# Kernel optimization log

Hardware: AMD Instinct MI355X
Metric: run time of the kernel (lower is better)

Reference implementation:

```python
import jax, jax.numpy as jnp
import numpy as np

ALPHA = 0.25
GAMMA = 2.0
VAR = jnp.array([0.1, 0.1, 0.2, 0.2, 0.1, 0.1, 0.2, 0.2], dtype=jnp.float32)


def calc_iou(a, b):
    # a: [A,4] anchors, b: [M,4] gt boxes -> IoU [A,M]
    area = (b[:, 2] - b[:, 0]) * (b[:, 3] - b[:, 1])
    iw = jnp.maximum(jnp.minimum(a[:, 2:3], b[:, 2]) - jnp.maximum(a[:, 0:1], b[:, 0]), 0.0)
    ih = jnp.maximum(jnp.minimum(a[:, 3:4], b[:, 3]) - jnp.maximum(a[:, 1:2], b[:, 1]), 0.0)
    ua = jnp.maximum(((a[:, 2] - a[:, 0]) * (a[:, 3] - a[:, 1]))[:, None] + area - iw * ih, 1e-8)
    return iw * ih / ua


def _per_sample(cls_p, reg, anchor, ann1, ann2):
    A = anchor.shape[0]
    M = ann1.shape[0]
    C = cls_p.shape[1]
    clsp = jnp.clip(cls_p, 1e-4, 1.0 - 1e-4)
    iou = calc_iou(anchor, ann1[:, :4])               # [A,M]
    bto = jnp.max(iou, axis=1)                        # best_truth_overlap [A]
    bti = jnp.argmax(iou, axis=1)                     # best_truth_idx [A]
    bpi = jnp.argmax(iou, axis=0)                     # best_prior_idx [M]
    bto = bto.at[bpi].set(2.0)
    owner = jnp.full((A,), -1, jnp.int32).at[bpi].max(jnp.arange(M, dtype=jnp.int32))
    bti = jnp.where(owner >= 0, owner, bti.astype(jnp.int32))
    pos = bto >= 0.5
    neg = bto < 0.4
    assigned = ann1[bti]                              # [A,6]
    labels = assigned[:, 4].astype(jnp.int32)
    onehot = jax.nn.one_hot(labels, C, dtype=clsp.dtype)
    targets = jnp.where(neg[:, None], 0.0, -1.0)
    targets = jnp.where(pos[:, None], onehot, targets)
    af = jnp.where(targets == 1.0, ALPHA, 1.0 - ALPHA)
    fw = af * jnp.where(targets == 1.0, 1.0 - clsp, clsp) ** GAMMA
    bce = -(targets * jnp.log(clsp) + (1.0 - targets) * jnp.log(1.0 - clsp))
    cls_loss = jnp.where(targets != -1.0, fw * bce, 0.0)
    npos = jnp.sum(pos).astype(clsp.dtype)
    cls_out = cls_loss.sum() / jnp.maximum(npos, 1.0)

    aw = anchor[:, 2] - anchor[:, 0]
    ah = anchor[:, 3] - anchor[:, 1]
    acx = anchor[:, 0] + 0.5 * aw
    acy = anchor[:, 1] + 0.5 * ah
    # track-id first-match between frames (replaces nested python loops)
    match = assigned[:, 5][:, None] == ann2[:, 5][None, :]   # [A,M2]
    has = jnp.any(match, axis=1)
    first = jnp.argmax(match, axis=1)
    ann_next = jnp.where(has[:, None], ann2[first], 0.0)     # [A,6]
    gw0 = assigned[:, 2] - assigned[:, 0]
    gh0 = assigned[:, 3] - assigned[:, 1]
    gcx = assigned[:, 0] + 0.5 * gw0
    gcy = assigned[:, 1] + 0.5 * gh0
    gw = jnp.maximum(gw0, 1.0)
    gh = jnp.maximum(gh0, 1.0)
    nw0 = ann_next[:, 2] - ann_next[:, 0]
    nh0 = ann_next[:, 3] - ann_next[:, 1]
    ncx = ann_next[:, 0] + 0.5 * nw0
    ncy = ann_next[:, 1] + 0.5 * nh0
    nw = jnp.maximum(nw0, 1.0)
    nh = jnp.maximum(nh0, 1.0)
    t = jnp.stack([
        (gcx - acx) / aw, (gcy - acy) / ah, jnp.log(gw / aw), jnp.log(gh / ah),
        (ncx - acx) / aw, (ncy - acy) / ah, jnp.log(nw / aw), jnp.log(nh / ah)
    ], axis=1) / VAR                                          # [A,8]
    reg_mask = jnp.concatenate([
        jnp.ones((A, 4), clsp.dtype),
        jnp.broadcast_to(has[:, None], (A, 4)).astype(clsp.dtype)
    ], axis=1)
    diff = jnp.abs(t - reg) * reg_mask
    hub = jnp.where(diff <= 1.0 / 9.0, 0.5 * 9.0 * diff ** 2, diff - 0.5 / 9.0)
    reg_out = jnp.sum(hub * pos[:, None].astype(clsp.dtype)) / jnp.maximum(npos * 8.0, 1.0)
    return cls_out, reg_out


def reference(classifications, regressions, anchors, annotations1, annotations2):
    cl, rl = jax.vmap(_per_sample, in_axes=(0, 0, None, 0, 0))(
        classifications, regressions, anchors[0], annotations1, annotations2)
    return jnp.mean(cl, keepdims=True), jnp.mean(rl, keepdims=True)


def setup_inputs() -> dict:
    key = jax.random.key(0)
    ks = jax.random.split(key, 10)
    B, A, C, M = 8, 100000, 80, 32
    IMG = 512.0

    def rand_boxes(k, prefix):
        k1, k2 = jax.random.split(k)
        ctr = jax.random.uniform(k1, prefix + (2,), jnp.float32, 0.0, IMG)
        wh = jax.random.uniform(k2, prefix + (2,), jnp.float32, 16.0, 128.0)
        return jnp.concatenate([ctr - 0.5 * wh, ctr + 0.5 * wh], axis=-1)

    anchors = rand_boxes(ks[0], (1, A))
    classifications = jax.random.uniform(ks[1], (B, A, C), jnp.float32)
    regressions = jax.random.normal(ks[2], (B, A, 8), jnp.float32) * 0.1

    def make_ann(kb, ki):
        boxes = rand_boxes(kb, (B, M))
        lbl = jax.random.randint(ki, (B, M, 1), 0, C).astype(jnp.float32)
        tid = jax.random.randint(jax.random.fold_in(ki, 1), (B, M, 1), 0, 40).astype(jnp.float32)
        return jnp.concatenate([boxes, lbl, tid], axis=-1)

    annotations1 = make_ann(ks[3], ks[4])
    annotations2 = make_ann(ks[5], ks[6])
    return {"classifications": classifications, "regressions": regressions,
            "anchors": anchors, "annotations1": annotations1, "annotations2": annotations2}
```

## Files before the change

kernel.cpp:

```cpp
#include <hip/hip_runtime.h>

typedef unsigned long long ull;
typedef float nvec4 __attribute__((ext_vector_type(4)));

#define MMAX 128

__global__ void k_init(ull* __restrict__ bpi, int* __restrict__ npos,
                       float* __restrict__ cls_sum, float* __restrict__ reg_sum,
                       int BM, int B) {
    int i = blockIdx.x * blockDim.x + threadIdx.x;
    if (i < BM) bpi[i] = 0ull;
    if (i < B) { npos[i] = 0; cls_sum[i] = 0.f; reg_sum[i] = 0.f; }
}

__global__ void k_iou(const float* __restrict__ anchors, const float* __restrict__ ann1,
                      float* __restrict__ bto, int* __restrict__ bti, ull* __restrict__ bpi,
                      int A, int M) {
    __shared__ float s_box[MMAX][4];
    __shared__ float s_area[MMAX];
    __shared__ ull s_part[4][MMAX];
    const int b = blockIdx.y;
    const int tid = threadIdx.x;
    for (int i = tid; i < M; i += blockDim.x) {
        const float* g = ann1 + ((size_t)b * M + i) * 6;
        float x1 = g[0], y1 = g[1], x2 = g[2], y2 = g[3];
        s_box[i][0] = x1; s_box[i][1] = y1; s_box[i][2] = x2; s_box[i][3] = y2;
        s_area[i] = (x2 - x1) * (y2 - y1);
    }
    __syncthreads();

    const int base = blockIdx.x * (blockDim.x * 4);
    float ax1[4], ay1[4], ax2[4], ay2[4], aar[4];
    int aidx[4]; bool val[4];
#pragma unroll
    for (int u = 0; u < 4; ++u) {
        int a = base + u * blockDim.x + tid;
        aidx[u] = a; val[u] = (a < A);
        float4 av = make_float4(0.f, 0.f, 0.f, 0.f);
        if (val[u]) av = ((const float4*)anchors)[a];
        ax1[u] = av.x; ay1[u] = av.y; ax2[u] = av.z; ay2[u] = av.w;
        aar[u] = (av.z - av.x) * (av.w - av.y);
    }
    float best[4] = {-1.f, -1.f, -1.f, -1.f};
    int bestj[4] = {0, 0, 0, 0};
    const int lane = tid & 63, wid = tid >> 6;

    for (int j = 0; j < M; ++j) {
        float bx1 = s_box[j][0], by1 = s_box[j][1], bx2 = s_box[j][2], by2 = s_box[j][3];
        float bar = s_area[j];
        ull key = 0ull;
#pragma unroll
        for (int u = 0; u < 4; ++u) {
            float iw = fmaxf(fminf(ax2[u], bx2) - fmaxf(ax1[u], bx1), 0.f);
            float ih = fmaxf(fminf(ay2[u], by2) - fmaxf(ay1[u], by1), 0.f);
            float inter = iw * ih;
            float ua = fmaxf(aar[u] + bar - inter, 1e-8f);
            float iou = inter / ua;
            if (val[u]) {
                if (iou > best[u]) { best[u] = iou; bestj[u] = j; }
                ull k2 = (((ull)__float_as_uint(iou)) << 32) | (ull)(0xFFFFFFFFu - (unsigned)aidx[u]);
                if (k2 > key) key = k2;
            }
        }
#pragma unroll
        for (int off = 32; off > 0; off >>= 1) {
            ull o = __shfl_down(key, off);
            if (o > key) key = o;
        }
        if (lane == 0) s_part[wid][j] = key;
    }
#pragma unroll
    for (int u = 0; u < 4; ++u) {
        if (val[u]) {
            bto[(size_t)b * A + aidx[u]] = best[u];
            bti[(size_t)b * A + aidx[u]] = bestj[u];
        }
    }
    __syncthreads();
    for (int j = tid; j < M; j += blockDim.x) {
        ull key = s_part[0][j];
        if (s_part[1][j] > key) key = s_part[1][j];
        if (s_part[2][j] > key) key = s_part[2][j];
        if (s_part[3][j] > key) key = s_part[3][j];
        atomicMax(&bpi[(size_t)b * M + j], key);
    }
}

__global__ void k_force(const ull* __restrict__ bpi, float* __restrict__ bto,
                        int* __restrict__ bti, int A, int M, int B) {
    int b = blockIdx.x * blockDim.x + threadIdx.x;
    if (b >= B) return;
    for (int j = 0; j < M; ++j) {
        ull key = bpi[(size_t)b * M + j];
        unsigned a = 0xFFFFFFFFu - (unsigned)(key & 0xFFFFFFFFull);
        bto[(size_t)b * A + a] = 2.0f;
        bti[(size_t)b * A + a] = j;
    }
}

template <int C4C>
__global__ void k_cls(const float* __restrict__ cls, const float* __restrict__ ann1,
                      const float* __restrict__ bto, const int* __restrict__ bti,
                      float* __restrict__ cls_sum, int A, int c4_rt, int M) {
    const int c4 = (C4C > 0) ? C4C : c4_rt;
    const int b = blockIdx.y;
    const int N4 = A * c4;
    const nvec4* cb = (const nvec4*)(cls + (size_t)b * A * (c4 * 4));
    const float* btob = bto + (size_t)b * A;
    const int* btib = bti + (size_t)b * A;
    const float* ann1b = ann1 + (size_t)b * M * 6;
    float lsum = 0.f;
    const int stride = gridDim.x * blockDim.x;
    for (int i = blockIdx.x * blockDim.x + threadIdx.x; i < N4; i += stride) {
        int a = i / c4;
        int c0 = (i - a * c4) * 4;
        float v = btob[a];
        bool pos = (v >= 0.5f), neg = (v < 0.4f);
        if (pos || neg) {
            nvec4 x = __builtin_nontemporal_load(&cb[i]);
            int label = -1;
            if (pos) label = (int)ann1b[btib[a] * 6 + 4];
            float xs[4] = {x[0], x[1], x[2], x[3]};
#pragma unroll
            for (int k = 0; k < 4; ++k) {
                float p = fminf(fmaxf(xs[k], 1e-4f), 1.0f - 1e-4f);
                if (pos && (c0 + k) == label) {
                    float q = 1.f - p;
                    lsum += 0.25f * q * q * (-__logf(p));
                } else {
                    lsum += 0.75f * p * p * (-__logf(1.f - p));
                }
            }
        }
    }
#pragma unroll
    for (int off = 32; off > 0; off >>= 1) lsum += __shfl_down(lsum, off);
    __shared__ float s_red[4];
    if ((threadIdx.x & 63) == 0) s_red[threadIdx.x >> 6] = lsum;
    __syncthreads();
    if (threadIdx.x == 0)
        atomicAdd(&cls_sum[b], s_red[0] + s_red[1] + s_red[2] + s_red[3]);
}

__global__ void k_reg(const float* __restrict__ anchors, const float* __restrict__ ann1,
                      const float* __restrict__ ann2, const float* __restrict__ regs,
                      const float* __restrict__ bto, const int* __restrict__ bti,
                      float* __restrict__ reg_sum, int* __restrict__ npos,
                      int A, int M, int M2) {
    __shared__ float s_a1[MMAX * 6];
    __shared__ float s_a2[MMAX * 6];
    const int b = blockIdx.y;
    const int tid = threadIdx.x;
    for (int i = tid; i < M * 6; i += blockDim.x) s_a1[i] = ann1[(size_t)b * M * 6 + i];
    for (int i = tid; i < M2 * 6; i += blockDim.x) s_a2[i] = ann2[(size_t)b * M2 * 6 + i];
    __syncthreads();

    const int a = blockIdx.x * blockDim.x + tid;
    float sum = 0.f;
    int cnt = 0;
    if (a < A) {
        float v = bto[(size_t)b * A + a];
        if (v >= 0.5f) {
            cnt = 1;
            const int ji = bti[(size_t)b * A + a];
            const float* as = &s_a1[ji * 6];
            float4 av = ((const float4*)anchors)[a];
            float aw = av.z - av.x, ah = av.w - av.y;
            float acx = av.x + 0.5f * aw, acy = av.y + 0.5f * ah;
            float gw0 = as[2] - as[0], gh0 = as[3] - as[1];
            float gcx = as[0] + 0.5f * gw0, gcy = as[1] + 0.5f * gh0;
            float gw = fmaxf(gw0, 1.f), gh = fmaxf(gh0, 1.f);
            float t[8];
            t[0] = ((gcx - acx) / aw) / 0.1f;
            t[1] = ((gcy - acy) / ah) / 0.1f;
            t[2] = __logf(gw / aw) / 0.2f;
            t[3] = __logf(gh / ah) / 0.2f;
            int nterm = 4;
            float tid5 = as[5];
            int first = -1;
            for (int j2 = 0; j2 < M2; ++j2) {
                if (s_a2[j2 * 6 + 5] == tid5) { first = j2; break; }
            }
            if (first >= 0) {
                const float* ns = &s_a2[first * 6];
                float nw0 = ns[2] - ns[0], nh0 = ns[3] - ns[1];
                float ncx = ns[0] + 0.5f * nw0, ncy = ns[1] + 0.5f * nh0;
                float nw = fmaxf(nw0, 1.f), nh = fmaxf(nh0, 1.f);
                t[4] = ((ncx - acx) / aw) / 0.1f;
                t[5] = ((ncy - acy) / ah) / 0.1f;
                t[6] = __logf(nw / aw) / 0.2f;
                t[7] = __logf(nh / ah) / 0.2f;
                nterm = 8;
            }
            const float* rg = regs + ((size_t)b * A + a) * 8;
            for (int k = 0; k < nterm; ++k) {
                float d = fabsf(t[k] - __builtin_nontemporal_load(&rg[k]));
                sum += (d <= (1.0f / 9.0f)) ? (4.5f * d * d) : (d - (0.5f / 9.0f));
            }
        }
    }
#pragma unroll
    for (int off = 32; off > 0; off >>= 1) {
        sum += __shfl_down(sum, off);
        cnt += __shfl_down(cnt, off);
    }
    __shared__ float s_rs[4];
    __shared__ int s_rc[4];
    if ((tid & 63) == 0) { s_rs[tid >> 6] = sum; s_rc[tid >> 6] = cnt; }
    __syncthreads();
    if (tid == 0) {
        atomicAdd(&reg_sum[b], s_rs[0] + s_rs[1] + s_rs[2] + s_rs[3]);
        atomicAdd(&npos[b], s_rc[0] + s_rc[1] + s_rc[2] + s_rc[3]);
    }
}

__global__ void k_final(const float* __restrict__ cls_sum, const float* __restrict__ reg_sum,
                        const int* __restrict__ npos, float* __restrict__ out, int B) {
    if (blockIdx.x == 0 && threadIdx.x == 0) {
        float c = 0.f, r = 0.f;
        for (int b = 0; b < B; ++b) {
            float np_ = (float)npos[b];
            c += cls_sum[b] / fmaxf(np_, 1.f);
            r += reg_sum[b] / fmaxf(np_ * 8.f, 1.f);
        }
        out[0] = c / (float)B;
        out[1] = r / (float)B;
    }
}

extern "C" void kernel_launch(void* const* d_in, const int* in_sizes, int n_in,
                              void* d_out, int out_size, void* d_ws, size_t ws_size,
                              hipStream_t stream) {
    const float* cls = (const float*)d_in[0];
    const float* regs = (const float*)d_in[1];
    const float* anchors = (const float*)d_in[2];
    const float* ann1 = (const float*)d_in[3];
    const float* ann2 = (const float*)d_in[4];
    float* out = (float*)d_out;

    const int A = in_sizes[2] / 4;
    const int B = in_sizes[1] / (A * 8);
    const int C = in_sizes[0] / (B * A);
    const int M = in_sizes[3] / (B * 6);
    const int M2 = in_sizes[4] / (B * 6);

    char* ws = (char*)d_ws;
    size_t off = 0;
    ull* bpi = (ull*)(ws + off);      off += (size_t)B * M * sizeof(ull);   off = (off + 255) & ~(size_t)255;
    int* npos = (int*)(ws + off);     off += (size_t)B * sizeof(int);       off = (off + 255) & ~(size_t)255;
    float* cls_sum = (float*)(ws + off); off += (size_t)B * sizeof(float);  off = (off + 255) & ~(size_t)255;
    float* reg_sum = (float*)(ws + off); off += (size_t)B * sizeof(float);  off = (off + 255) & ~(size_t)255;
    float* bto = (float*)(ws + off);  off += (size_t)B * A * sizeof(float); off = (off + 255) & ~(size_t)255;
    int* bti = (int*)(ws + off);      off += (size_t)B * A * sizeof(int);

    int initN = (B * M > B) ? B * M : B;
    k_init<<<dim3((initN + 255) / 256), dim3(256), 0, stream>>>(bpi, npos, cls_sum, reg_sum, B * M, B);

    dim3 g1((A + 1023) / 1024, B);
    k_iou<<<g1, dim3(256), 0, stream>>>(anchors, ann1, bto, bti, bpi, A, M);

    k_force<<<dim3(1), dim3(64), 0, stream>>>(bpi, bto, bti, A, M, B);

    dim3 g3(512, B);
    if (C % 4 == 0 && C / 4 == 20)
        k_cls<20><<<g3, dim3(256), 0, stream>>>(cls, ann1, bto, bti, cls_sum, A, C / 4, M);
    else
        k_cls<0><<<g3, dim3(256), 0, stream>>>(cls, ann1, bto, bti, cls_sum, A, C / 4, M);

    dim3 g4((A + 255) / 256, B);
    k_reg<<<g4, dim3(256), 0, stream>>>(anchors, ann1, ann2, regs, bto, bti, reg_sum, npos, A, M, M2);

    k_final<<<1, 1, 0, stream>>>(cls_sum, reg_sum, npos, out, B);
}
```

Baseline: 478.0 us.

## Fuse force, cls, reg and final kernels using last-block completion counters

Folds the single-thread force-match step into the tail of the IoU kernel via a per-batch last-block atomic counter, and handles duplicate anchors by having each gt check later gts instead of writing serially. The classification and regression kernels are merged into one launch with a flattened grid, and the final reduction runs in the last finishing block. This removes three kernel launches and the serial k_force, at the cost of extra atomics and threadfences.

Result: slower. 1.201 ms (+151.3%).

```diff
diff --git a/kernel.cpp b/kernel.cpp
--- a/kernel.cpp
+++ b/kernel.cpp
@@ -5,17 +5,19 @@
 
 #define MMAX 128
 
-__global__ void k_init(ull* __restrict__ bpi, int* __restrict__ npos,
+__global__ void k_init(ull* __restrict__ bpi, int* __restrict__ cnt1,
                        float* __restrict__ cls_sum, float* __restrict__ reg_sum,
+                       int* __restrict__ npos, int* __restrict__ cnt2,
                        int BM, int B) {
-    int i = blockIdx.x * blockDim.x + threadIdx.x;
-    if (i < BM) bpi[i] = 0ull;
-    if (i < B) { npos[i] = 0; cls_sum[i] = 0.f; reg_sum[i] = 0.f; }
+    int tid = threadIdx.x;
+    for (int i = tid; i < BM; i += blockDim.x) bpi[i] = 0ull;
+    if (tid < B) { cnt1[tid] = 0; cls_sum[tid] = 0.f; reg_sum[tid] = 0.f; npos[tid] = 0; }
+    if (tid == 0) cnt2[0] = 0;
 }
 
 __global__ void k_iou(const float* __restrict__ anchors, const float* __restrict__ ann1,
                       float* __restrict__ bto, int* __restrict__ bti, ull* __restrict__ bpi,
-                      int A, int M) {
+                      int* __restrict__ cnt1, int A, int M) {
     __shared__ float s_box[MMAX][4];
     __shared__ float s_area[MMAX];
     __shared__ ull s_part[4][MMAX];
@@ -84,147 +86,167 @@
         if (s_part[3][j] > key) key = s_part[3][j];
         atomicMax(&bpi[(size_t)b * M + j], key);
     }
-}
-
-__global__ void k_force(const ull* __restrict__ bpi, float* __restrict__ bto,
-                        int* __restrict__ bti, int A, int M, int B) {
-    int b = blockIdx.x * blockDim.x + threadIdx.x;
-    if (b >= B) return;
-    for (int j = 0; j < M; ++j) {
-        ull key = bpi[(size_t)b * M + j];
-        unsigned a = 0xFFFFFFFFu - (unsigned)(key & 0xFFFFFFFFull);
-        bto[(size_t)b * A + a] = 2.0f;
-        bti[(size_t)b * A + a] = j;
+
+    __threadfence();
+    __shared__ int s_last;
+    if (tid == 0) s_last = (atomicAdd(&cnt1[b], 1) == (int)gridDim.x - 1) ? 1 : 0;
+    __syncthreads();
+    if (s_last) {
+        __shared__ unsigned s_fa[MMAX];
+        if (tid < M) {
+            ull key = atomicMax(&bpi[(size_t)b * M + tid], 0ull);
+            s_fa[tid] = 0xFFFFFFFFu - (unsigned)(key & 0xFFFFFFFFull);
+        }
+        __syncthreads();
+        if (tid < M) {
+            unsigned a = s_fa[tid];
+            bool win = true;
+            for (int j2 = tid + 1; j2 < M; ++j2)
+                if (s_fa[j2] == a) { win = false; break; }
+            if (win) {
+                bto[(size_t)b * A + a] = 2.0f;
+                bti[(size_t)b * A + a] = tid;
+            }
+        }
     }
 }
 
 template <int C4C>
-__global__ void k_cls(const float* __restrict__ cls, const float* __restrict__ ann1,
-                      const float* __restrict__ bto, const int* __restrict__ bti,
-                      float* __restrict__ cls_sum, int A, int c4_rt, int M) {
+__global__ void k_main(const float* __restrict__ cls, const float* __restrict__ regs,
+                       const float* __restrict__ anchors, const float* __restrict__ ann1,
+                       const float* __restrict__ ann2,
+                       const float* __restrict__ bto, const int* __restrict__ bti,
+                       float* __restrict__ cls_sum, float* __restrict__ reg_sum,
+                       int* __restrict__ npos, int* __restrict__ cnt2,
+                       float* __restrict__ out,
+                       int A, int c4_rt, int M, int M2, int B, int NBC, int NBR) {
     const int c4 = (C4C > 0) ? C4C : c4_rt;
-    const int b = blockIdx.y;
-    const int N4 = A * c4;
-    const nvec4* cb = (const nvec4*)(cls + (size_t)b * A * (c4 * 4));
-    const float* btob = bto + (size_t)b * A;
-    const int* btib = bti + (size_t)b * A;
-    const float* ann1b = ann1 + (size_t)b * M * 6;
-    float lsum = 0.f;
-    const int stride = gridDim.x * blockDim.x;
-    for (int i = blockIdx.x * blockDim.x + threadIdx.x; i < N4; i += stride) {
-        int a = i / c4;
-        int c0 = (i - a * c4) * 4;
-        float v = btob[a];
-        bool pos = (v >= 0.5f), neg = (v < 0.4f);
-        if (pos || neg) {
-            nvec4 x = __builtin_nontemporal_load(&cb[i]);
-            int label = -1;
-            if (pos) label = (int)ann1b[btib[a] * 6 + 4];
-            float xs[4] = {x[0], x[1], x[2], x[3]};
-#pragma unroll
-            for (int k = 0; k < 4; ++k) {
-                float p = fminf(fmaxf(xs[k], 1e-4f), 1.0f - 1e-4f);
-                if (pos && (c0 + k) == label) {
-                    float q = 1.f - p;
-                    lsum += 0.25f * q * q * (-__logf(p));
-                } else {
-                    lsum += 0.75f * p * p * (-__logf(1.f - p));
-                }
-            }
-        }
-    }
-#pragma unroll
-    for (int off = 32; off > 0; off >>= 1) lsum += __shfl_down(lsum, off);
-    __shared__ float s_red[4];
-    if ((threadIdx.x & 63) == 0) s_red[threadIdx.x >> 6] = lsum;
-    __syncthreads();
-    if (threadIdx.x == 0)
-        atomicAdd(&cls_sum[b], s_red[0] + s_red[1] + s_red[2] + s_red[3]);
-}
-
-__global__ void k_reg(const float* __restrict__ anchors, const float* __restrict__ ann1,
-                      const float* __restrict__ ann2, const float* __restrict__ regs,
-                      const float* __restrict__ bto, const int* __restrict__ bti,
-                      float* __restrict__ reg_sum, int* __restrict__ npos,
-                      int A, int M, int M2) {
+    const int bid = blockIdx.x;
+    const int tid = threadIdx.x;
     __shared__ float s_a1[MMAX * 6];
     __shared__ float s_a2[MMAX * 6];
-    const int b = blockIdx.y;
-    const int tid = threadIdx.x;
-    for (int i = tid; i < M * 6; i += blockDim.x) s_a1[i] = ann1[(size_t)b * M * 6 + i];
-    for (int i = tid; i < M2 * 6; i += blockDim.x) s_a2[i] = ann2[(size_t)b * M2 * 6 + i];
-    __syncthreads();
-
-    const int a = blockIdx.x * blockDim.x + tid;
-    float sum = 0.f;
-    int cnt = 0;
-    if (a < A) {
-        float v = bto[(size_t)b * A + a];
-        if (v >= 0.5f) {
-            cnt = 1;
-            const int ji = bti[(size_t)b * A + a];
-            const float* as = &s_a1[ji * 6];
-            float4 av = ((const float4*)anchors)[a];
-            float aw = av.z - av.x, ah = av.w - av.y;
-            float acx = av.x + 0.5f * aw, acy = av.y + 0.5f * ah;
-            float gw0 = as[2] - as[0], gh0 = as[3] - as[1];
-            float gcx = as[0] + 0.5f * gw0, gcy = as[1] + 0.5f * gh0;
-            float gw = fmaxf(gw0, 1.f), gh = fmaxf(gh0, 1.f);
-            float t[8];
-            t[0] = ((gcx - acx) / aw) / 0.1f;
-            t[1] = ((gcy - acy) / ah) / 0.1f;
-            t[2] = __logf(gw / aw) / 0.2f;
-            t[3] = __logf(gh / ah) / 0.2f;
-            int nterm = 4;
-            float tid5 = as[5];
-            int first = -1;
-            for (int j2 = 0; j2 < M2; ++j2) {
-                if (s_a2[j2 * 6 + 5] == tid5) { first = j2; break; }
-            }
-            if (first >= 0) {
-                const float* ns = &s_a2[first * 6];
-                float nw0 = ns[2] - ns[0], nh0 = ns[3] - ns[1];
-                float ncx = ns[0] + 0.5f * nw0, ncy = ns[1] + 0.5f * nh0;
-                float nw = fmaxf(nw0, 1.f), nh = fmaxf(nh0, 1.f);
-                t[4] = ((ncx - acx) / aw) / 0.1f;
-                t[5] = ((ncy - acy) / ah) / 0.1f;
-                t[6] = __logf(nw / aw) / 0.2f;
-                t[7] = __logf(nh / ah) / 0.2f;
-                nterm = 8;
-            }
-            const float* rg = regs + ((size_t)b * A + a) * 8;
-            for (int k = 0; k < nterm; ++k) {
-                float d = fabsf(t[k] - __builtin_nontemporal_load(&rg[k]));
-                sum += (d <= (1.0f / 9.0f)) ? (4.5f * d * d) : (d - (0.5f / 9.0f));
-            }
-        }
-    }
-#pragma unroll
-    for (int off = 32; off > 0; off >>= 1) {
-        sum += __shfl_down(sum, off);
-        cnt += __shfl_down(cnt, off);
-    }
-    __shared__ float s_rs[4];
-    __shared__ int s_rc[4];
-    if ((tid & 63) == 0) { s_rs[tid >> 6] = sum; s_rc[tid >> 6] = cnt; }
-    __syncthreads();
-    if (tid == 0) {
-        atomicAdd(&reg_sum[b], s_rs[0] + s_rs[1] + s_rs[2] + s_rs[3]);
-        atomicAdd(&npos[b], s_rc[0] + s_rc[1] + s_rc[2] + s_rc[3]);
-    }
-}
-
-__global__ void k_final(const float* __restrict__ cls_sum, const float* __restrict__ reg_sum,
-                        const int* __restrict__ npos, float* __restrict__ out, int B) {
-    if (blockIdx.x == 0 && threadIdx.x == 0) {
-        float c = 0.f, r = 0.f;
-        for (int b = 0; b < B; ++b) {
-            float np_ = (float)npos[b];
-            c += cls_sum[b] / fmaxf(np_, 1.f);
-            r += reg_sum[b] / fmaxf(np_ * 8.f, 1.f);
+    __shared__ float s_red[4];
+    __shared__ int s_redi[4];
+
+    if (bid < B * NBC) {
+        const int b = bid / NBC;
+        const int xb = bid - b * NBC;
+        const int N4 = A * c4;
+        const nvec4* cb = (const nvec4*)(cls + (size_t)b * A * (c4 * 4));
+        const float* btob = bto + (size_t)b * A;
+        const int* btib = bti + (size_t)b * A;
+        const float* ann1b = ann1 + (size_t)b * M * 6;
+        float lsum = 0.f;
+        const int stride = NBC * blockDim.x;
+        for (int i = xb * blockDim.x + tid; i < N4; i += stride) {
+            int a = i / c4;
+            int c0 = (i - a * c4) * 4;
+            float v = btob[a];
+            bool pos = (v >= 0.5f), neg = (v < 0.4f);
+            if (pos || neg) {
+                nvec4 x = __builtin_nontemporal_load(&cb[i]);
+                int label = -1;
+                if (pos) label = (int)ann1b[btib[a] * 6 + 4];
+                float xs[4] = {x[0], x[1], x[2], x[3]};
+#pragma unroll
+                for (int k = 0; k < 4; ++k) {
+                    float p = fminf(fmaxf(xs[k], 1e-4f), 1.0f - 1e-4f);
+                    if (pos && (c0 + k) == label) {
+                        float q = 1.f - p;
+                        lsum += 0.25f * q * q * (-__logf(p));
+                    } else {
+                        lsum += 0.75f * p * p * (-__logf(1.f - p));
+                    }
+                }
+            }
+        }
+#pragma unroll
+        for (int off = 32; off > 0; off >>= 1) lsum += __shfl_down(lsum, off);
+        if ((tid & 63) == 0) s_red[tid >> 6] = lsum;
+        __syncthreads();
+        if (tid == 0)
+            atomicAdd(&cls_sum[b], s_red[0] + s_red[1] + s_red[2] + s_red[3]);
+    } else {
+        const int r = bid - B * NBC;
+        const int b = r / NBR;
+        const int xb = r - b * NBR;
+        for (int i = tid; i < M * 6; i += blockDim.x) s_a1[i] = ann1[(size_t)b * M * 6 + i];
+        for (int i = tid; i < M2 * 6; i += blockDim.x) s_a2[i] = ann2[(size_t)b * M2 * 6 + i];
+        __syncthreads();
+
+        const int a = xb * blockDim.x + tid;
+        float sum = 0.f;
+        int cnt = 0;
+        if (a < A) {
+            float v = bto[(size_t)b * A + a];
+            if (v >= 0.5f) {
+                cnt = 1;
+                const int ji = bti[(size_t)b * A + a];
+                const float* as = &s_a1[ji * 6];
+                float4 av = ((const float4*)anchors)[a];
+                float aw = av.z - av.x, ah = av.w - av.y;
+                float acx = av.x + 0.5f * aw, acy = av.y + 0.5f * ah;
+                float gw0 = as[2] - as[0], gh0 = as[3] - as[1];
+                float gcx = as[0] + 0.5f * gw0, gcy = as[1] + 0.5f * gh0;
+                float gw = fmaxf(gw0, 1.f), gh = fmaxf(gh0, 1.f);
+                float t[8];
+                t[0] = ((gcx - acx) / aw) / 0.1f;
+                t[1] = ((gcy - acy) / ah) / 0.1f;
+                t[2] = __logf(gw / aw) / 0.2f;
+                t[3] = __logf(gh / ah) / 0.2f;
+                int nterm = 4;
+                float tid5 = as[5];
+                int first = -1;
+                for (int j2 = 0; j2 < M2; ++j2) {
+                    if (s_a2[j2 * 6 + 5] == tid5) { first = j2; break; }
+                }
+                if (first >= 0) {
+                    const float* ns = &s_a2[first * 6];
+                    float nw0 = ns[2] - ns[0], nh0 = ns[3] - ns[1];
+                    float ncx = ns[0] + 0.5f * nw0, ncy = ns[1] + 0.5f * nh0;
+                    float nw = fmaxf(nw0, 1.f), nh = fmaxf(nh0, 1.f);
+                    t[4] = ((ncx - acx) / aw) / 0.1f;
+                    t[5] = ((ncy - acy) / ah) / 0.1f;
+                    t[6] = __logf(nw / aw) / 0.2f;
+                    t[7] = __logf(nh / ah) / 0.2f;
+                    nterm = 8;
+                }
+                const float* rg = regs + ((size_t)b * A + a) * 8;
+                for (int k = 0; k < nterm; ++k) {
+                    float d = fabsf(t[k] - __builtin_nontemporal_load(&rg[k]));
+                    sum += (d <= (1.0f / 9.0f)) ? (4.5f * d * d) : (d - (0.5f / 9.0f));
+                }
+            }
+        }
+#pragma unroll
+        for (int off = 32; off > 0; off >>= 1) {
+            sum += __shfl_down(sum, off);
+            cnt += __shfl_down(cnt, off);
+        }
+        if ((tid & 63) == 0) { s_red[tid >> 6] = sum; s_redi[tid >> 6] = cnt; }
+        __syncthreads();
+        if (tid == 0) {
+            atomicAdd(&reg_sum[b], s_red[0] + s_red[1] + s_red[2] + s_red[3]);
+            atomicAdd(&npos[b], s_redi[0] + s_redi[1] + s_redi[2] + s_redi[3]);
+        }
+    }
+
+    __threadfence();
+    __shared__ int s_win;
+    if (tid == 0) s_win = (atomicAdd(cnt2, 1) == (int)gridDim.x - 1) ? 1 : 0;
+    __syncthreads();
+    if (s_win && tid == 0) {
+        float c = 0.f, rr = 0.f;
+        for (int b2 = 0; b2 < B; ++b2) {
+            float cs = atomicAdd(&cls_sum[b2], 0.f);
+            float rs = atomicAdd(&reg_sum[b2], 0.f);
+            int np = atomicAdd(&npos[b2], 0);
+            float npf = (float)np;
+            c += cs / fmaxf(npf, 1.f);
+            rr += rs / fmaxf(npf * 8.f, 1.f);
         }
         out[0] = c / (float)B;
-        out[1] = r / (float)B;
+        out[1] = rr / (float)B;
     }
 }
 
@@ -247,28 +269,28 @@
     char* ws = (char*)d_ws;
     size_t off = 0;
     ull* bpi = (ull*)(ws + off);      off += (size_t)B * M * sizeof(ull);   off = (off + 255) & ~(size_t)255;
-    int* npos = (int*)(ws + off);     off += (size_t)B * sizeof(int);       off = (off + 255) & ~(size_t)255;
+    int* cnt1 = (int*)(ws + off);     off += (size_t)B * sizeof(int);       off = (off + 255) & ~(size_t)255;
     float* cls_sum = (float*)(ws + off); off += (size_t)B * sizeof(float);  off = (off + 255) & ~(size_t)255;
     float* reg_sum = (float*)(ws + off); off += (size_t)B * sizeof(float);  off = (off + 255) & ~(size_t)255;
+    int* npos = (int*)(ws + off);     off += (size_t)B * sizeof(int);       off = (off + 255) & ~(size_t)255;
+    int* cnt2 = (int*)(ws + off);     off += 256;
     float* bto = (float*)(ws + off);  off += (size_t)B * A * sizeof(float); off = (off + 255) & ~(size_t)255;
     int* bti = (int*)(ws + off);      off += (size_t)B * A * sizeof(int);
 
-    int initN = (B * M > B) ? B * M : B;
-    k_init<<<dim3((initN + 255) / 256), dim3(256), 0, stream>>>(bpi, npos, cls_sum, reg_sum, B * M, B);
+    k_init<<<dim3(1), dim3(512), 0, stream>>>(bpi, cnt1, cls_sum, reg_sum, npos, cnt2, B * M, B);
 
     dim3 g1((A + 1023) / 1024, B);
-    k_iou<<<g1, dim3(256), 0, stream>>>(anchors, ann1, bto, bti, bpi, A, M);
-
-    k_force<<<dim3(1), dim3(64), 0, stream>>>(bpi, bto, bti, A, M, B);
-
-    dim3 g3(512, B);
+    k_iou<<<g1, dim3(256), 0, stream>>>(anchors, ann1, bto, bti, bpi, cnt1, A, M);
+
+    const int NBC = 512;
+    const int NBR = (A + 255) / 256;
+    dim3 g2(B * (NBC + NBR));
     if (C % 4 == 0 && C / 4 == 20)
-        k_cls<20><<<g3, dim3(256), 0, stream>>>(cls, ann1, bto, bti, cls_sum, A, C / 4, M);
+        k_main<20><<<g2, dim3(256), 0, stream>>>(cls, regs, anchors, ann1, ann2, bto, bti,
+                                                 cls_sum, reg_sum, npos, cnt2, out,
+                                                 A, C / 4, M, M2, B, NBC, NBR);
     else
-        k_cls<0><<<g3, dim3(256), 0, stream>>>(cls, ann1, bto, bti, cls_sum, A, C / 4, M);
-
-    dim3 g4((A + 255) / 256, B);
-    k_reg<<<g4, dim3(256), 0, stream>>>(anchors, ann1, ann2, regs, bto, bti, reg_sum, npos, A, M, M2);
-
-    k_final<<<1, 1, 0, stream>>>(cls_sum, reg_sum, npos, out, B);
-}
+        k_main<0><<<g2, dim3(256), 0, stream>>>(cls, regs, anchors, ann1, ann2, bto, bti,
+                                                cls_sum, reg_sum, npos, cnt2, out,
+                                                A, C / 4, M, M2, B, NBC, NBR);
+}
```

## Tile classification loss per anchor block, parallelize force step, drop nontemporal loads

Applied to the files above, without the earlier changes.

The classification kernel now handles a 128-anchor tile per block. It first decodes each anchor's pos/neg/label into a shared-memory code, so the per-element loop no longer re-reads bto, bti and ann1. The grid grows from a fixed 512×B grid-stride layout to one block per tile. The force-match step now runs one thread per (batch, gt) and uses a shared-memory scan to keep last-write-wins semantics, replacing a serial loop. Nontemporal loads are swapped for plain loads in both the classification and regression kernels. A launch of dim3(M,B) assumes M*B stays within the block-size limit and B≤16.

Measured after the change: 482.8 us. Within noise of the previous version (+1.0%).

```diff
diff --git a/kernel.cpp b/kernel.cpp
--- a/kernel.cpp
+++ b/kernel.cpp
@@ -1,9 +1,10 @@
 #include <hip/hip_runtime.h>
 
 typedef unsigned long long ull;
-typedef float nvec4 __attribute__((ext_vector_type(4)));
 
 #define MMAX 128
+#define BMAX 16
+#define TILE 128
 
 __global__ void k_init(ull* __restrict__ bpi, int* __restrict__ npos,
                        float* __restrict__ cls_sum, float* __restrict__ reg_sum,
@@ -88,11 +89,17 @@
 
 __global__ void k_force(const ull* __restrict__ bpi, float* __restrict__ bto,
                         int* __restrict__ bti, int A, int M, int B) {
-    int b = blockIdx.x * blockDim.x + threadIdx.x;
-    if (b >= B) return;
-    for (int j = 0; j < M; ++j) {
-        ull key = bpi[(size_t)b * M + j];
-        unsigned a = 0xFFFFFFFFu - (unsigned)(key & 0xFFFFFFFFull);
+    __shared__ unsigned s_fa[BMAX][MMAX];
+    const int j = threadIdx.x;
+    const int b = threadIdx.y;
+    ull key = bpi[(size_t)b * M + j];
+    unsigned a = 0xFFFFFFFFu - (unsigned)(key & 0xFFFFFFFFull);
+    s_fa[b][j] = a;
+    __syncthreads();
+    bool win = true;
+    for (int j2 = j + 1; j2 < M; ++j2)
+        if (s_fa[b][j2] == a) { win = false; break; }
+    if (win) {
         bto[(size_t)b * A + a] = 2.0f;
         bti[(size_t)b * A + a] = j;
     }
@@ -104,41 +111,56 @@
                       float* __restrict__ cls_sum, int A, int c4_rt, int M) {
     const int c4 = (C4C > 0) ? C4C : c4_rt;
     const int b = blockIdx.y;
-    const int N4 = A * c4;
-    const nvec4* cb = (const nvec4*)(cls + (size_t)b * A * (c4 * 4));
-    const float* btob = bto + (size_t)b * A;
-    const int* btib = bti + (size_t)b * A;
-    const float* ann1b = ann1 + (size_t)b * M * 6;
+    const int tid = threadIdx.x;
+    const int base_a = blockIdx.x * TILE;
+    __shared__ int s_code[TILE];
+    __shared__ float s_red[4];
+
+    if (tid < TILE) {
+        int a = base_a + tid;
+        int code = -2;
+        if (a < A) {
+            float v = bto[(size_t)b * A + a];
+            if (v >= 0.5f)
+                code = (int)ann1[((size_t)b * M + bti[(size_t)b * A + a]) * 6 + 4];
+            else if (v < 0.4f)
+                code = -1;
+        }
+        s_code[tid] = code;
+    }
+    __syncthreads();
+
+    const float4* cb = (const float4*)(cls + (size_t)b * A * (c4 * 4));
     float lsum = 0.f;
-    const int stride = gridDim.x * blockDim.x;
-    for (int i = blockIdx.x * blockDim.x + threadIdx.x; i < N4; i += stride) {
-        int a = i / c4;
-        int c0 = (i - a * c4) * 4;
-        float v = btob[a];
-        bool pos = (v >= 0.5f), neg = (v < 0.4f);
-        if (pos || neg) {
-            nvec4 x = __builtin_nontemporal_load(&cb[i]);
-            int label = -1;
-            if (pos) label = (int)ann1b[btib[a] * 6 + 4];
-            float xs[4] = {x[0], x[1], x[2], x[3]};
-#pragma unroll
-            for (int k = 0; k < 4; ++k) {
-                float p = fminf(fmaxf(xs[k], 1e-4f), 1.0f - 1e-4f);
-                if (pos && (c0 + k) == label) {
-                    float q = 1.f - p;
-                    lsum += 0.25f * q * q * (-__logf(p));
-                } else {
-                    lsum += 0.75f * p * p * (-__logf(1.f - p));
+    const int nf4 = TILE * c4;
+    for (int i = tid; i < nf4; i += 256) {
+        int al = i / c4;
+        int f = i - al * c4;
+        int a = base_a + al;
+        if (a < A) {
+            int code = s_code[al];
+            if (code != -2) {
+                float4 x = cb[(size_t)a * c4 + f];
+                int c0 = f * 4;
+                float xs[4] = {x.x, x.y, x.z, x.w};
+#pragma unroll
+                for (int k = 0; k < 4; ++k) {
+                    float p = fminf(fmaxf(xs[k], 1e-4f), 1.0f - 1e-4f);
+                    if (code == c0 + k) {
+                        float q = 1.f - p;
+                        lsum += 0.25f * q * q * (-__logf(p));
+                    } else {
+                        lsum += 0.75f * p * p * (-__logf(1.f - p));
+                    }
                 }
             }
         }
     }
 #pragma unroll
     for (int off = 32; off > 0; off >>= 1) lsum += __shfl_down(lsum, off);
-    __shared__ float s_red[4];
-    if ((threadIdx.x & 63) == 0) s_red[threadIdx.x >> 6] = lsum;
-    __syncthreads();
-    if (threadIdx.x == 0)
+    if ((tid & 63) == 0) s_red[tid >> 6] = lsum;
+    __syncthreads();
+    if (tid == 0)
         atomicAdd(&cls_sum[b], s_red[0] + s_red[1] + s_red[2] + s_red[3]);
 }
 
@@ -194,7 +216,7 @@
             }
             const float* rg = regs + ((size_t)b * A + a) * 8;
             for (int k = 0; k < nterm; ++k) {
-                float d = fabsf(t[k] - __builtin_nontemporal_load(&rg[k]));
+                float d = fabsf(t[k] - rg[k]);
                 sum += (d <= (1.0f / 9.0f)) ? (4.5f * d * d) : (d - (0.5f / 9.0f));
             }
         }
@@ -259,9 +281,9 @@
     dim3 g1((A + 1023) / 1024, B);
     k_iou<<<g1, dim3(256), 0, stream>>>(anchors, ann1, bto, bti, bpi, A, M);
 
-    k_force<<<dim3(1), dim3(64), 0, stream>>>(bpi, bto, bti, A, M, B);
-
-    dim3 g3(512, B);
+    k_force<<<dim3(1), dim3(M, B), 0, stream>>>(bpi, bto, bti, A, M, B);
+
+    dim3 g3((A + TILE - 1) / TILE, B);
     if (C % 4 == 0 && C / 4 == 20)
         k_cls<20><<<g3, dim3(256), 0, stream>>>(cls, ann1, bto, bti, cls_sum, A, C / 4, M);
     else
```
